# Optimization experiments

Hardware: AMD Instinct MI355X
Metric: run time of the kernel (lower is better)

Reference implementation:

```python
import jax, jax.numpy as jnp
import numpy as np

MIN_FP16 = -65504.0  # torch.finfo(torch.float16).min
D_MODEL = 2048
NUM_HEAD = 16
HEAD_SIZE = D_MODEL // NUM_HEAD


def setup_inputs() -> dict:
    key = jax.random.key(0)
    k1, k2, k3, k4, k5 = jax.random.split(key, 5)
    B, S, D = 4, 2048, D_MODEL
    scale_in = 1.0 / np.sqrt(D)
    return {
        "x": jax.random.normal(k1, (B, S, D), dtype=jnp.float32),
        # nn.Linear(d_model, 3*d_model): weight [3D, D], bias [3D]
        "w_proj": jax.random.normal(k2, (3 * D, D), dtype=jnp.float32) * scale_in,
        "b_proj": jax.random.normal(k3, (3 * D,), dtype=jnp.float32) * 0.01,
        # nn.Linear(d_model, d_model)
        "w_ff": jax.random.normal(k4, (D, D), dtype=jnp.float32) * scale_in,
        "b_ff": jax.random.normal(k5, (D,), dtype=jnp.float32) * 0.01,
    }


def reference(x, w_proj, b_proj, w_ff, b_ff):
    B, S, D = x.shape
    H, hs = NUM_HEAD, HEAD_SIZE
    # fused QKV projection: [B,S,3D]
    x_proj = jnp.einsum("bsd,ed->bse", x, w_proj) + b_proj
    # view [B,S,H,3*hs] -> [B,H,S,3*hs], split into q,k,v [B,H,S,hs]
    x_proj = x_proj.reshape(B, S, H, 3 * hs).transpose(0, 2, 1, 3)
    q, k, v = jnp.split(x_proj, 3, axis=-1)
    next_prefix_kv = jnp.stack((k, v))  # [2,B,H,S,hs]
    # scaled scores [B,H,S,S]
    scores = jnp.einsum("bhqd,bhkd->bhqk", q, k) / np.sqrt(hs)
    # causal mask (prefix_kv=None => tmp_len == seq_len, offset 0)
    causal = jnp.tril(jnp.ones((S, S), dtype=bool))
    scores = jnp.where(causal, scores, MIN_FP16)
    probs = jax.nn.softmax(scores, axis=-1)  # dropout p=0 (eval)
    attn_o = jnp.einsum("bhqk,bhkd->bhqd", probs, v)
    attn_o = attn_o.transpose(0, 2, 1, 3).reshape(B, S, D)
    ff_o = jnp.einsum("bsd,ed->bse", attn_o, w_ff) + b_ff
    return ff_o, next_prefix_kv
```

## Files before the change

### kernel.cpp

```cpp
#include <hip/hip_runtime.h>


using floatx4 = __attribute__((ext_vector_type(4))) float;
using short8  = __attribute__((ext_vector_type(8))) short;

#define MFMA_BF16(a, b, c) __builtin_amdgcn_mfma_f32_16x16x32_bf16((a), (b), (c), 0, 0, 0)

static __device__ __forceinline__ unsigned short f2bf(float f) {
    unsigned u = __float_as_uint(f);
    u += 0x7FFF + ((u >> 16) & 1);
    return (unsigned short)(u >> 16);
}
static __device__ __forceinline__ short8 cvt8(const float* p) {
    float4 a = ((const float4*)p)[0];
    float4 b = ((const float4*)p)[1];
    short8 r;
    r[0] = (short)f2bf(a.x); r[1] = (short)f2bf(a.y);
    r[2] = (short)f2bf(a.z); r[3] = (short)f2bf(a.w);
    r[4] = (short)f2bf(b.x); r[5] = (short)f2bf(b.y);
    r[6] = (short)f2bf(b.z); r[7] = (short)f2bf(b.w);
    return r;
}

static __device__ __forceinline__ void gld16(const void* g, const void* l) {
    unsigned loff = (unsigned)__builtin_amdgcn_readfirstlane((int)(unsigned)(uintptr_t)l);
    __builtin_amdgcn_global_load_lds(
        (__attribute__((address_space(1))) unsigned*)(uintptr_t)g,
        (__attribute__((address_space(3))) unsigned*)loff,
        16, 0, 0);
}

__global__ __launch_bounds__(256) void cvt_kernel(
    const float* __restrict__ X, const float* __restrict__ Wp,
    const float* __restrict__ Wf,
    unsigned short* __restrict__ Xb, unsigned short* __restrict__ Wpb,
    unsigned short* __restrict__ Wfb, int doWf)
{
    const int NX = 2097152;
    const int NP = 1572864;
    const int NF = 524288;
    const int total = NX + NP + (doWf ? NF : 0);
    const int stride = gridDim.x * 256;
    for (int g = blockIdx.x * 256 + threadIdx.x; g < total; g += stride) {
        const float* src; unsigned short* dst; int off;
        if (g < NX)           { src = X;  dst = Xb;  off = g; }
        else if (g < NX + NP) { src = Wp; dst = Wpb; off = g - NX; }
        else                  { src = Wf; dst = Wfb; off = g - NX - NP; }
        const int row = off >> 8;
        const int c   = off & 255;
        const int dof = (row << 8) | (c & ~7) | ((c ^ row) & 7);
        short8 v = cvt8(src + (size_t)off * 8);
        *(short8*)(dst + (size_t)dof * 8) = v;
    }
}

__global__ __launch_bounds__(256) void gemm_qkv_kernel(
    const unsigned short* __restrict__ Xb,
    const unsigned short* __restrict__ Wpb,
    const float* __restrict__ Bias,
    unsigned short* __restrict__ Qws,
    float* __restrict__ KV)
{
    const int K = 2048;
    __shared__ unsigned short As[128 * 64];
    __shared__ unsigned short Bs[128 * 64];
    const int n0 = blockIdx.x * 128;
    const int m0 = blockIdx.y * 128;
    const int t = threadIdx.x;
    const int w = t >> 6, l = t & 63;
    const int lr = l & 15, lq = l >> 4;
    const int lr7 = lr & 7;
    const int wr = w >> 1, wc = w & 1;
    const int srow = l >> 3;
    const int scol = (l & 7) * 8;

    floatx4 acc[4][4];
#pragma unroll
    for (int mi = 0; mi < 4; ++mi)
#pragma unroll
        for (int ni = 0; ni < 4; ++ni) acc[mi][ni] = (floatx4){0, 0, 0, 0};

    for (int k0 = 0; k0 < K; k0 += 64) {
        __syncthreads();
#pragma unroll
        for (int i = 0; i < 4; ++i) {
            const int rb = (i * 4 + w) * 8;
            gld16(Xb  + (size_t)(m0 + rb + srow) * K + k0 + scol, &As[(rb)*64]);
            gld16(Wpb + (size_t)(n0 + rb + srow) * K + k0 + scol, &Bs[(rb)*64]);
        }
        __syncthreads();
#pragma unroll
        for (int kc = 0; kc < 2; ++kc) {
            short8 af[4], bg[4];
#pragma unroll
            for (int mi = 0; mi < 4; ++mi)
                af[mi] = *(const short8*)
                    &As[(wr * 64 + mi * 16 + lr) * 64 + ((((kc << 2) | lq) ^ lr7) << 3)];
#pragma unroll
            for (int ni = 0; ni < 4; ++ni)
                bg[ni] = *(const short8*)
                    &Bs[(wc * 64 + ni * 16 + lr) * 64 + ((((kc << 2) | lq) ^ lr7) << 3)];
#pragma unroll
            for (int mi = 0; mi < 4; ++mi)
#pragma unroll
                for (int ni = 0; ni < 4; ++ni)
                    acc[mi][ni] = MFMA_BF16(af[mi], bg[ni], acc[mi][ni]);
        }
    }
#pragma unroll
    for (int ni = 0; ni < 4; ++ni) {
        int e = n0 + wc * 64 + ni * 16 + lr;
        int h = e / 384;
        int c = e - h * 384;
        float bias = Bias[e];
#pragma unroll
        for (int mi = 0; mi < 4; ++mi) {
#pragma unroll
            for (int r = 0; r < 4; ++r) {
                int m = m0 + wr * 64 + mi * 16 + lq * 4 + r;
                int b = m >> 11, s = m & 2047;
                float o = acc[mi][ni][r] + bias;
                size_t base = (((size_t)(b * 16 + h)) * 2048 + s) * 128;
                if (c < 128)
                    Qws[base + ((((c >> 3) ^ (s & 7)) << 3) | (c & 7))] = f2bf(o);
                else if (c < 256) KV[base + (c - 128)] = o;
                else              KV[(size_t)16777216 + base + (c - 256)] = o;
            }
        }
    }
}

__global__ __launch_bounds__(256) void repack_kv_kernel(
    const float* __restrict__ KV,
    unsigned short* __restrict__ Kb,
    unsigned short* __restrict__ Vtb)
{
    __shared__ short Vt[128][72];
    const int bh = blockIdx.x >> 5;
    const int w  = blockIdx.x & 31;
    const int t  = threadIdx.x;

    {
        const int kr = t >> 2;
        const int c4 = (t & 3) * 4;
        const int s  = w * 64 + kr;
        const float* kp = KV + ((size_t)bh * 2048 + s) * 128 + c4 * 8;
        unsigned short* ko = Kb + ((size_t)bh * 2048 + s) * 128;
        const int sw = s & 7;
#pragma unroll
        for (int j = 0; j < 4; ++j) {
            short8 v = cvt8(kp + j * 8);
            *(short8*)(ko + ((c4 + j) ^ sw) * 8) = v;
        }
    }

    {
        const int vkp = t & 31;
        const int vd0 = (t >> 5) * 16;
        const float* vap = KV + (((size_t)64 + bh) * 2048 + w * 64 + 2 * vkp) * 128 + vd0;
        short8 va0 = cvt8(vap),       va1 = cvt8(vap + 8);
        short8 vb0 = cvt8(vap + 128), vb1 = cvt8(vap + 136);
#pragma unroll
        for (int dd = 0; dd < 8; ++dd) {
            unsigned w0 = (unsigned)(unsigned short)va0[dd] |
                          ((unsigned)(unsigned short)vb0[dd] << 16);
            unsigned w1 = (unsigned)(unsigned short)va1[dd] |
                          ((unsigned)(unsigned short)vb1[dd] << 16);
            *(unsigned*)&Vt[vd0 + dd][2 * vkp]     = w0;
            *(unsigned*)&Vt[vd0 + 8 + dd][2 * vkp] = w1;
        }
    }
    __syncthreads();
    {
        const int d = t >> 1, hf = t & 1;
        unsigned short* vo = Vtb + ((size_t)bh * 128 + d) * 2048 + w * 64;
        const int dw = d & 7;
#pragma unroll
        for (int j = 0; j < 4; ++j) {
            int c = hf * 4 + j;
            uint4 v = *(const uint4*)&Vt[d][c * 8];
            *(uint4*)(vo + (c ^ dw) * 8) = v;
        }
    }
}

__global__ __launch_bounds__(256) void attn_kernel(
    unsigned short* __restrict__ QA,
    const unsigned short* __restrict__ Kb,
    const unsigned short* __restrict__ Vtb)
{
    const int S = 2048;
    __shared__ unsigned short Ks[64 * 128];
    __shared__ unsigned short Vt[128 * 64];
    __shared__ short Pb[4][16][72];

    const int bh = blockIdx.y;
    const int qt = gridDim.x - 1 - blockIdx.x;
    const int q0 = qt * 64;
    const int t = threadIdx.x;
    const int wv = t >> 6;
    const int l = t & 63;
    const int lr = l & 15;
    const int lq = l >> 4;
    const int lr7 = lr & 7;

    unsigned short* Qp = QA + ((size_t)bh * S + q0) * 128;
    const unsigned short* gK = Kb + (size_t)bh * S * 128;
    const unsigned short* gV = Vtb + (size_t)bh * 128 * S;

    short8 qf[4];
#pragma unroll
    for (int kc = 0; kc < 4; ++kc)
        qf[kc] = *(const short8*)(Qp + (size_t)(wv * 16 + lr) * 128 +
                                  ((((kc << 2) | lq) ^ lr7) << 3));

    float m_i = -1e30f, l_i = 0.0f;
    floatx4 oacc[8];
#pragma unroll
    for (int nt = 0; nt < 8; ++nt) oacc[nt] = (floatx4){0, 0, 0, 0};

    const int ntiles = qt + 1;
    for (int it = 0; it < ntiles; ++it) {
        const int kv0 = it * 64;
        __syncthreads();
#pragma unroll
        for (int i = 0; i < 4; ++i) {
            const int off = (i * 16 + wv * 4) * 128;
            gld16(gK + (size_t)kv0 * 128 + off + l * 8, &Ks[off]);
        }
#pragma unroll
        for (int i = 0; i < 4; ++i) {
            const int ob = (i * 16 + wv * 4) * 256 + l * 16;
            const int d = ob >> 7, rem = ob & 127;
            gld16((const char*)gV + (size_t)d * (S * 2) + kv0 * 2 + rem,
                  (const char*)Vt + (i * 16 + wv * 4) * 256);
        }
        __syncthreads();

        floatx4 sacc[4];
#pragma unroll
        for (int mt = 0; mt < 4; ++mt) sacc[mt] = (floatx4){0, 0, 0, 0};
#pragma unroll
        for (int kc = 0; kc < 4; ++kc) {
#pragma unroll
            for (int mt = 0; mt < 4; ++mt) {
                short8 a = *(const short8*)
                    &Ks[(mt * 16 + lr) * 128 + ((((kc << 2) | lq) ^ lr7) << 3)];
                sacc[mt] = MFMA_BF16(a, qf[kc], sacc[mt]);
            }
        }

        float sv[16];
        const bool diag = (it == qt);
#pragma unroll
        for (int mt = 0; mt < 4; ++mt)
#pragma unroll
            for (int r = 0; r < 4; ++r) {
                float x = sacc[mt][r] * 0.08838834764831845f;
                if (diag && (mt * 16 + lq * 4 + r > wv * 16 + lr)) x = -1e30f;
                sv[mt * 4 + r] = x;
            }
        float mx = sv[0];
#pragma unroll
        for (int j = 1; j < 16; ++j) mx = fmaxf(mx, sv[j]);
        mx = fmaxf(mx, __shfl_xor(mx, 16));
        mx = fmaxf(mx, __shfl_xor(mx, 32));
        float m_new = fmaxf(m_i, mx);
        float alpha = __expf(m_i - m_new);
        m_i = m_new;
        float sum = 0.0f;
        unsigned pw[8];
#pragma unroll
        for (int j = 0; j < 8; ++j) {
            float p0 = __expf(sv[2 * j]     - m_new);
            float p1 = __expf(sv[2 * j + 1] - m_new);
            sum += p0 + p1;
            pw[j] = (unsigned)f2bf(p0) | ((unsigned)f2bf(p1) << 16);
        }
        sum += __shfl_xor(sum, 16);
        sum += __shfl_xor(sum, 32);
        l_i = l_i * alpha + sum;

#pragma unroll
        for (int mt = 0; mt < 4; ++mt)
            *(uint2*)&Pb[wv][lr][mt * 16 + lq * 4] =
                make_uint2(pw[2 * mt], pw[2 * mt + 1]);

        float am[4];
#pragma unroll
        for (int r = 0; r < 4; ++r) am[r] = __shfl(alpha, lq * 4 + r);
#pragma unroll
        for (int nt = 0; nt < 8; ++nt)
#pragma unroll
            for (int r = 0; r < 4; ++r) oacc[nt][r] *= am[r];

        short8 pa0 = *(const short8*)&Pb[wv][lr][lq * 8];
        short8 pa1 = *(const short8*)&Pb[wv][lr][32 + lq * 8];
#pragma unroll
        for (int nt = 0; nt < 8; ++nt) {
            const int row = nt * 16 + lr;
            short8 v0 = *(const short8*)&Vt[row * 64 + ((lq ^ lr7) << 3)];
            short8 v1 = *(const short8*)&Vt[row * 64 + (((4 + lq) ^ lr7) << 3)];
            oacc[nt] = MFMA_BF16(pa0, v0, oacc[nt]);
            oacc[nt] = MFMA_BF16(pa1, v1, oacc[nt]);
        }
    }

    float lm[4];
#pragma unroll
    for (int r = 0; r < 4; ++r) lm[r] = 1.0f / __shfl(l_i, lq * 4 + r);
#pragma unroll
    for (int nt = 0; nt < 8; ++nt) {
#pragma unroll
        for (int r = 0; r < 4; ++r) {
            int q = wv * 16 + lq * 4 + r;
            int ch = (nt * 2 + (lr >> 3)) ^ (q & 7);
            Qp[(size_t)q * 128 + (ch << 3) + (lr & 7)] = f2bf(oacc[nt][r] * lm[r]);
        }
    }
}

__global__ __launch_bounds__(256) void gemm_ff_kernel(
    const unsigned short* __restrict__ AOhm,
    const unsigned short* __restrict__ Wfb,
    const float* __restrict__ Bias,
    float* __restrict__ Out)
{
    const int K = 2048;
    __shared__ unsigned short As[128 * 64];
    __shared__ unsigned short Bs[128 * 64];
    const int n0 = blockIdx.x * 128;
    const int m0 = blockIdx.y * 128;
    const int t = threadIdx.x;
    const int w = t >> 6, l = t & 63;
    const int lr = l & 15, lq = l >> 4;
    const int lr7 = lr & 7;
    const int wr = w >> 1, wc = w & 1;
    const int srow = l >> 3;
    const int scol = (l & 7) * 8;

    floatx4 acc[4][4];
#pragma unroll
    for (int mi = 0; mi < 4; ++mi)
#pragma unroll
        for (int ni = 0; ni < 4; ++ni) acc[mi][ni] = (floatx4){0, 0, 0, 0};

    for (int k0 = 0; k0 < K; k0 += 64) {
        const int h = k0 >> 7, d0 = (k0 & 127) + scol;
        __syncthreads();
#pragma unroll
        for (int i = 0; i < 4; ++i) {
            const int rb = (i * 4 + w) * 8;
            const int m = m0 + rb + srow;
            const int b = m >> 11, s = m & 2047;
            gld16(AOhm + ((size_t)(b * 16 + h) * 2048 + s) * 128 + d0, &As[(rb)*64]);
            gld16(Wfb  + (size_t)(n0 + rb + srow) * K + k0 + scol,     &Bs[(rb)*64]);
        }
        __syncthreads();
#pragma unroll
        for (int kc = 0; kc < 2; ++kc) {
            short8 af[4], bg[4];
#pragma unroll
            for (int mi = 0; mi < 4; ++mi)
                af[mi] = *(const short8*)
                    &As[(wr * 64 + mi * 16 + lr) * 64 + ((((kc << 2) | lq) ^ lr7) << 3)];
#pragma unroll
            for (int ni = 0; ni < 4; ++ni)
                bg[ni] = *(const short8*)
                    &Bs[(wc * 64 + ni * 16 + lr) * 64 + ((((kc << 2) | lq) ^ lr7) << 3)];
#pragma unroll
            for (int mi = 0; mi < 4; ++mi)
#pragma unroll
                for (int ni = 0; ni < 4; ++ni)
                    acc[mi][ni] = MFMA_BF16(af[mi], bg[ni], acc[mi][ni]);
        }
    }
#pragma unroll
    for (int ni = 0; ni < 4; ++ni) {
        int e = n0 + wc * 64 + ni * 16 + lr;
        float bias = Bias[e];
#pragma unroll
        for (int mi = 0; mi < 4; ++mi) {
#pragma unroll
            for (int r = 0; r < 4; ++r) {
                int m = m0 + wr * 64 + mi * 16 + lq * 4 + r;
                Out[(size_t)m * 2048 + e] = acc[mi][ni][r] + bias;
            }
        }
    }
}

__global__ __launch_bounds__(256) void gemm_ff_fb_kernel(
    const unsigned short* __restrict__ AOhm,
    const float* __restrict__ W,
    const float* __restrict__ Bias,
    float* __restrict__ Out)
{
    const int K = 2048;
    __shared__ short As[64][72];
    __shared__ short Bs[64][72];
    const int n0 = blockIdx.x * 64;
    const int m0 = blockIdx.y * 64;
    const int t = threadIdx.x;
    const int wv = t >> 6;
    const int l = t & 63;
    const int lr = l & 15;
    const int lq = l >> 4;
    const int srow = t >> 2;
    const int scol = (t & 3) << 4;

    floatx4 acc[4] = {{0,0,0,0},{0,0,0,0},{0,0,0,0},{0,0,0,0}};

    const int mrow = m0 + srow;
    const int b = mrow >> 11, s = mrow & 2047;
    const int sw = s & 7;
    const unsigned short* gA = AOhm + (size_t)(b * 16) * 262144 + (size_t)s * 128;
    const float* gB = W + (size_t)(n0 + srow) * K + scol;

    for (int k0 = 0; k0 < K; k0 += 64) {
        int kk = k0 + scol;
        int h = kk >> 7, d = kk & 127;
        int span = (d >> 6) * 64;
        int c0 = (d >> 3) & 7;
        const unsigned short* pa = gA + (size_t)h * 262144 + span;
        uint4 av0 = *(const uint4*)(pa + ((c0 ^ sw) << 3));
        uint4 av1 = *(const uint4*)(pa + (((c0 + 1) ^ sw) << 3));
        short8 b0 = cvt8(gB + k0);
        short8 b1 = cvt8(gB + k0 + 8);
        __syncthreads();
        *(uint4*)&As[srow][scol]      = av0;
        *(uint4*)&As[srow][scol + 8]  = av1;
        *(short8*)&Bs[srow][scol]     = b0;
        *(short8*)&Bs[srow][scol + 8] = b1;
        __syncthreads();
#pragma unroll
        for (int kc = 0; kc < 2; ++kc) {
            short8 a = *(const short8*)&As[wv * 16 + lr][kc * 32 + lq * 8];
#pragma unroll
            for (int j = 0; j < 4; ++j) {
                short8 b2 = *(const short8*)&Bs[j * 16 + lr][kc * 32 + lq * 8];
                acc[j] = MFMA_BF16(a, b2, acc[j]);
            }
        }
    }
#pragma unroll
    for (int j = 0; j < 4; ++j) {
        int e = n0 + j * 16 + lr;
        float bias = Bias[e];
#pragma unroll
        for (int r = 0; r < 4; ++r) {
            int m = m0 + wv * 16 + lq * 4 + r;
            Out[(size_t)m * 2048 + e] = acc[j][r] + bias;
        }
    }
}

extern "C" void kernel_launch(void* const* d_in, const int* in_sizes, int n_in,
                              void* d_out, int out_size, void* d_ws, size_t ws_size,
                              hipStream_t stream) {
    const float* X  = (const float*)d_in[0];
    const float* Wp = (const float*)d_in[1];
    const float* bp = (const float*)d_in[2];
    const float* Wf = (const float*)d_in[3];
    const float* bf = (const float*)d_in[4];

    float* out = (float*)d_out;
    float* kv  = out + 16777216;
    unsigned short* Qws = (unsigned short*)d_ws;

    unsigned short* Xb  = (unsigned short*)out;
    unsigned short* Wpb = Xb + 16777216;
    unsigned short* Kbs = (unsigned short*)out;
    unsigned short* Vtb = Kbs + 16777216;
    const bool wfInWs = ws_size >= (size_t)33554432 + 8388608;
    unsigned short* Wfb = wfInWs ? Qws + 16777216 : (unsigned short*)nullptr;

    cvt_kernel<<<dim3(2048), 256, 0, stream>>>(X, Wp, Wf, Xb, Wpb, Wfb,
                                               wfInWs ? 1 : 0);
    gemm_qkv_kernel<<<dim3(48, 64), 256, 0, stream>>>(Xb, Wpb, bp, Qws, kv);
    repack_kv_kernel<<<dim3(2048), 256, 0, stream>>>(kv, Kbs, Vtb);
    attn_kernel<<<dim3(32, 64), 256, 0, stream>>>(Qws, Kbs, Vtb);
    if (wfInWs)
        gemm_ff_kernel<<<dim3(16, 64), 256, 0, stream>>>(Qws, Wfb, bf, out);
    else
        gemm_ff_fb_kernel<<<dim3(32, 128), 256, 0, stream>>>(Qws, Wf, bf, out);
}
```

Measured before the change: 1.091 ms.

## Double-buffer K/V tiles in attention and convert Wff inline in FF GEMM

The attention kernel now keeps two LDS buffers for K and V and prefetches the next tile with async global-to-LDS loads while the current tile is computed, dropping one barrier per iteration. The FF GEMM no longer uses a pre-converted bf16 weight copy. It loads fp32 W rows, converts them to bf16 in registers and writes them swizzled into LDS, which removes the Wf pass from cvt_kernel and the workspace-size fallback path. The attention prefetch relies on the barrier at the top of the next iteration for completion and doubles LDS use. The FF kernel now reads twice as many weight bytes per tile and does the conversion inside the GEMM loop.

```diff
diff --git a/kernel.cpp b/kernel.cpp
--- a/kernel.cpp
+++ b/kernel.cpp
@@ -32,20 +32,16 @@
 
 __global__ __launch_bounds__(256) void cvt_kernel(
     const float* __restrict__ X, const float* __restrict__ Wp,
-    const float* __restrict__ Wf,
-    unsigned short* __restrict__ Xb, unsigned short* __restrict__ Wpb,
-    unsigned short* __restrict__ Wfb, int doWf)
+    unsigned short* __restrict__ Xb, unsigned short* __restrict__ Wpb)
 {
     const int NX = 2097152;
     const int NP = 1572864;
-    const int NF = 524288;
-    const int total = NX + NP + (doWf ? NF : 0);
+    const int total = NX + NP;
     const int stride = gridDim.x * 256;
     for (int g = blockIdx.x * 256 + threadIdx.x; g < total; g += stride) {
         const float* src; unsigned short* dst; int off;
-        if (g < NX)           { src = X;  dst = Xb;  off = g; }
-        else if (g < NX + NP) { src = Wp; dst = Wpb; off = g - NX; }
-        else                  { src = Wf; dst = Wfb; off = g - NX - NP; }
+        if (g < NX) { src = X;  dst = Xb;  off = g; }
+        else        { src = Wp; dst = Wpb; off = g - NX; }
         const int row = off >> 8;
         const int c   = off & 255;
         const int dof = (row << 8) | (c & ~7) | ((c ^ row) & 7);
@@ -190,8 +186,8 @@
     const unsigned short* __restrict__ Vtb)
 {
     const int S = 2048;
-    __shared__ unsigned short Ks[64 * 128];
-    __shared__ unsigned short Vt[128 * 64];
+    __shared__ unsigned short Ks[2][64 * 128];
+    __shared__ unsigned short Vt[2][128 * 64];
     __shared__ short Pb[4][16][72];
 
     const int bh = blockIdx.y;
@@ -220,22 +216,33 @@
     for (int nt = 0; nt < 8; ++nt) oacc[nt] = (floatx4){0, 0, 0, 0};
 
     const int ntiles = qt + 1;
+
+#define STAGE(BUF, KV0)                                                        \
+    {                                                                          \
+        const int kv0_ = (KV0);                                                \
+        _Pragma("unroll")                                                      \
+        for (int i = 0; i < 4; ++i) {                                          \
+            const int off = (i * 16 + wv * 4) * 128;                           \
+            gld16(gK + (size_t)kv0_ * 128 + off + l * 8, &Ks[BUF][off]);       \
+        }                                                                      \
+        _Pragma("unroll")                                                      \
+        for (int i = 0; i < 4; ++i) {                                          \
+            const int ob = (i * 16 + wv * 4) * 256 + l * 16;                   \
+            const int d = ob >> 7, rem = ob & 127;                             \
+            gld16((const char*)gV + (size_t)d * (S * 2) + kv0_ * 2 + rem,      \
+                  (const char*)&Vt[BUF][0] + (i * 16 + wv * 4) * 256);         \
+        }                                                                      \
+    }
+
+    STAGE(0, 0);
+
     for (int it = 0; it < ntiles; ++it) {
-        const int kv0 = it * 64;
+        const int cur = it & 1;
         __syncthreads();
-#pragma unroll
-        for (int i = 0; i < 4; ++i) {
-            const int off = (i * 16 + wv * 4) * 128;
-            gld16(gK + (size_t)kv0 * 128 + off + l * 8, &Ks[off]);
-        }
-#pragma unroll
-        for (int i = 0; i < 4; ++i) {
-            const int ob = (i * 16 + wv * 4) * 256 + l * 16;
-            const int d = ob >> 7, rem = ob & 127;
-            gld16((const char*)gV + (size_t)d * (S * 2) + kv0 * 2 + rem,
-                  (const char*)Vt + (i * 16 + wv * 4) * 256);
-        }
-        __syncthreads();
+        if (it + 1 < ntiles) STAGE(cur ^ 1, (it + 1) * 64);
+
+        const unsigned short* Kc = &Ks[cur][0];
+        const unsigned short* Vc = &Vt[cur][0];
 
         floatx4 sacc[4];
 #pragma unroll
@@ -245,7 +252,7 @@
 #pragma unroll
             for (int mt = 0; mt < 4; ++mt) {
                 short8 a = *(const short8*)
-                    &Ks[(mt * 16 + lr) * 128 + ((((kc << 2) | lq) ^ lr7) << 3)];
+                    &Kc[(mt * 16 + lr) * 128 + ((((kc << 2) | lq) ^ lr7) << 3)];
                 sacc[mt] = MFMA_BF16(a, qf[kc], sacc[mt]);
             }
         }
@@ -299,12 +306,13 @@
 #pragma unroll
         for (int nt = 0; nt < 8; ++nt) {
             const int row = nt * 16 + lr;
-            short8 v0 = *(const short8*)&Vt[row * 64 + ((lq ^ lr7) << 3)];
-            short8 v1 = *(const short8*)&Vt[row * 64 + (((4 + lq) ^ lr7) << 3)];
+            short8 v0 = *(const short8*)&Vc[row * 64 + ((lq ^ lr7) << 3)];
+            short8 v1 = *(const short8*)&Vc[row * 64 + (((4 + lq) ^ lr7) << 3)];
             oacc[nt] = MFMA_BF16(pa0, v0, oacc[nt]);
             oacc[nt] = MFMA_BF16(pa1, v1, oacc[nt]);
         }
     }
+#undef STAGE
 
     float lm[4];
 #pragma unroll
@@ -322,7 +330,7 @@
 
 __global__ __launch_bounds__(256) void gemm_ff_kernel(
     const unsigned short* __restrict__ AOhm,
-    const unsigned short* __restrict__ Wfb,
+    const float* __restrict__ W,
     const float* __restrict__ Bias,
     float* __restrict__ Out)
 {
@@ -339,6 +347,11 @@
     const int srow = l >> 3;
     const int scol = (l & 7) * 8;
 
+    const int brow = t >> 1;
+    const int bch0 = (t & 1) * 4;
+    const int bsw  = brow & 7;
+    const float* gB = W + (size_t)(n0 + brow) * K + bch0 * 8;
+
     floatx4 acc[4][4];
 #pragma unroll
     for (int mi = 0; mi < 4; ++mi)
@@ -346,6 +359,10 @@
         for (int ni = 0; ni < 4; ++ni) acc[mi][ni] = (floatx4){0, 0, 0, 0};
 
     for (int k0 = 0; k0 < K; k0 += 64) {
+        short8 bc[4];
+#pragma unroll
+        for (int j = 0; j < 4; ++j) bc[j] = cvt8(gB + k0 + j * 8);
+
         const int h = k0 >> 7, d0 = (k0 & 127) + scol;
         __syncthreads();
 #pragma unroll
@@ -354,8 +371,10 @@
             const int m = m0 + rb + srow;
             const int b = m >> 11, s = m & 2047;
             gld16(AOhm + ((size_t)(b * 16 + h) * 2048 + s) * 128 + d0, &As[(rb)*64]);
-            gld16(Wfb  + (size_t)(n0 + rb + srow) * K + k0 + scol,     &Bs[(rb)*64]);
-        }
+        }
+#pragma unroll
+        for (int j = 0; j < 4; ++j)
+            *(short8*)&Bs[brow * 64 + (((bch0 + j) ^ bsw) << 3)] = bc[j];
         __syncthreads();
 #pragma unroll
         for (int kc = 0; kc < 2; ++kc) {
@@ -386,71 +405,6 @@
                 int m = m0 + wr * 64 + mi * 16 + lq * 4 + r;
                 Out[(size_t)m * 2048 + e] = acc[mi][ni][r] + bias;
             }
-        }
-    }
-}
-
-__global__ __launch_bounds__(256) void gemm_ff_fb_kernel(
-    const unsigned short* __restrict__ AOhm,
-    const float* __restrict__ W,
-    const float* __restrict__ Bias,
-    float* __restrict__ Out)
-{
-    const int K = 2048;
-    __shared__ short As[64][72];
-    __shared__ short Bs[64][72];
-    const int n0 = blockIdx.x * 64;
-    const int m0 = blockIdx.y * 64;
-    const int t = threadIdx.x;
-    const int wv = t >> 6;
-    const int l = t & 63;
-    const int lr = l & 15;
-    const int lq = l >> 4;
-    const int srow = t >> 2;
-    const int scol = (t & 3) << 4;
-
-    floatx4 acc[4] = {{0,0,0,0},{0,0,0,0},{0,0,0,0},{0,0,0,0}};
-
-    const int mrow = m0 + srow;
-    const int b = mrow >> 11, s = mrow & 2047;
-    const int sw = s & 7;
-    const unsigned short* gA = AOhm + (size_t)(b * 16) * 262144 + (size_t)s * 128;
-    const float* gB = W + (size_t)(n0 + srow) * K + scol;
-
-    for (int k0 = 0; k0 < K; k0 += 64) {
-        int kk = k0 + scol;
-        int h = kk >> 7, d = kk & 127;
-        int span = (d >> 6) * 64;
-        int c0 = (d >> 3) & 7;
-        const unsigned short* pa = gA + (size_t)h * 262144 + span;
-        uint4 av0 = *(const uint4*)(pa + ((c0 ^ sw) << 3));
-        uint4 av1 = *(const uint4*)(pa + (((c0 + 1) ^ sw) << 3));
-        short8 b0 = cvt8(gB + k0);
-        short8 b1 = cvt8(gB + k0 + 8);
-        __syncthreads();
-        *(uint4*)&As[srow][scol]      = av0;
-        *(uint4*)&As[srow][scol + 8]  = av1;
-        *(short8*)&Bs[srow][scol]     = b0;
-        *(short8*)&Bs[srow][scol + 8] = b1;
-        __syncthreads();
-#pragma unroll
-        for (int kc = 0; kc < 2; ++kc) {
-            short8 a = *(const short8*)&As[wv * 16 + lr][kc * 32 + lq * 8];
-#pragma unroll
-            for (int j = 0; j < 4; ++j) {
-                short8 b2 = *(const short8*)&Bs[j * 16 + lr][kc * 32 + lq * 8];
-                acc[j] = MFMA_BF16(a, b2, acc[j]);
-            }
-        }
-    }
-#pragma unroll
-    for (int j = 0; j < 4; ++j) {
-        int e = n0 + j * 16 + lr;
-        float bias = Bias[e];
-#pragma unroll
-        for (int r = 0; r < 4; ++r) {
-            int m = m0 + wv * 16 + lq * 4 + r;
-            Out[(size_t)m * 2048 + e] = acc[j][r] + bias;
         }
     }
 }
@@ -472,16 +426,10 @@
     unsigned short* Wpb = Xb + 16777216;
     unsigned short* Kbs = (unsigned short*)out;
     unsigned short* Vtb = Kbs + 16777216;
-    const bool wfInWs = ws_size >= (size_t)33554432 + 8388608;
-    unsigned short* Wfb = wfInWs ? Qws + 16777216 : (unsigned short*)nullptr;
-
-    cvt_kernel<<<dim3(2048), 256, 0, stream>>>(X, Wp, Wf, Xb, Wpb, Wfb,
-                                               wfInWs ? 1 : 0);
+
+    cvt_kernel<<<dim3(2048), 256, 0, stream>>>(X, Wp, Xb, Wpb);
     gemm_qkv_kernel<<<dim3(48, 64), 256, 0, stream>>>(Xb, Wpb, bp, Qws, kv);
     repack_kv_kernel<<<dim3(2048), 256, 0, stream>>>(kv, Kbs, Vtb);
     attn_kernel<<<dim3(32, 64), 256, 0, stream>>>(Qws, Kbs, Vtb);
-    if (wfInWs)
-        gemm_ff_kernel<<<dim3(16, 64), 256, 0, stream>>>(Qws, Wfb, bf, out);
-    else
-        gemm_ff_fb_kernel<<<dim3(32, 128), 256, 0, stream>>>(Qws, Wf, bf, out);
-}
+    gemm_ff_kernel<<<dim3(16, 64), 256, 0, stream>>>(Qws, Wf, bf, out);
+}
```

Result: faster. 962.4 us (-11.8%).
